# Kernel tuning notes

Measured on AMD Instinct MI355X. Metric: run time of the kernel, lower is better.

## Reference

```python
import jax, jax.numpy as jnp
import numpy as np

N_NODES = 100000
N_EDGES = 1600000


def gcn_conv(x, W, b, src, dst, n):
    # PyG GCNConv: x @ W, add self-loops, symmetric deg^{-1/2} normalization,
    # sum-aggregate messages from src into dst, then add bias.
    h = x @ W  # [N, out]
    loops = jnp.arange(n, dtype=src.dtype)
    s = jnp.concatenate([src, loops])
    d = jnp.concatenate([dst, loops])
    deg = jax.ops.segment_sum(jnp.ones_like(d, dtype=h.dtype), d, num_segments=n)
    dinv = 1.0 / jnp.sqrt(deg)  # deg >= 1 thanks to self-loops
    norm = dinv[s] * dinv[d]  # [E + N]
    msg = h[s] * norm[:, None]
    out = jax.ops.segment_sum(msg, d, num_segments=n)
    return out + b


def setup_inputs() -> dict:
    key = jax.random.key(0)
    k1, k2, k3, k4 = jax.random.split(key, 4)
    x = jax.random.normal(k1, (N_NODES, 64), dtype=jnp.float32)
    edge_index = jax.random.randint(k2, (2, N_EDGES), 0, N_NODES, dtype=jnp.int64)
    W1 = jax.random.normal(k3, (64, 32), dtype=jnp.float32) * (1.0 / np.sqrt(64))
    b1 = jnp.zeros((32,), dtype=jnp.float32)
    W2 = jax.random.normal(k4, (32, 16), dtype=jnp.float32) * (1.0 / np.sqrt(32))
    b2 = jnp.zeros((16,), dtype=jnp.float32)
    return {"x": x, "edge_index": edge_index, "W1": W1, "b1": b1, "W2": W2, "b2": b2}


def reference(x, edge_index, W1, b1, W2, b2):
    n = x.shape[0]
    src, dst = edge_index[0], edge_index[1]
    h = gcn_conv(x, W1, b1, src, dst, n)
    h = jax.nn.relu(h)
    h = gcn_conv(h, W2, b2, src, dst, n)
    return jax.nn.log_softmax(h, axis=1)
```

## Files before the change

### kernel.cpp

```cpp
#include <hip/hip_runtime.h>
#include <hip/hip_bf16.h>


#define FEAT_IN 64
#define FEAT_H  32
#define FEAT_O  16
#define MAXNB   512
#define PART_G  192

__global__ void k_detect(const uint4* __restrict__ xw4,
                         const int* __restrict__ ei, int* __restrict__ flags) {
    __shared__ int s_f32, s_i64nz;
    if (threadIdx.x == 0) { s_f32 = 0; s_i64nz = 0; }
    __syncthreads();
    int t = threadIdx.x;
    int hit = 0;
    for (int i = t; i < 4096; i += 256) {
        uint4 u = xw4[i];
        unsigned a0 = u.x, a1 = u.y, a2 = u.z, a3 = u.w;
        if ((a0 & 0x7F800000u) == 0x7F800000u || (a0 & 0x00007F80u) == 0x00007F80u) hit = 1;
        if ((a1 & 0x7F800000u) == 0x7F800000u || (a1 & 0x00007F80u) == 0x00007F80u) hit = 1;
        if ((a2 & 0x7F800000u) == 0x7F800000u || (a2 & 0x00007F80u) == 0x00007F80u) hit = 1;
        if ((a3 & 0x7F800000u) == 0x7F800000u || (a3 & 0x00007F80u) == 0x00007F80u) hit = 1;
    }
    if (hit) atomicOr(&s_f32, 1);
    int nz = 0;
    for (int i = t; i < 128; i += 256) {
        if (ei[2 * i + 1] != 0) nz = 1;
    }
    if (nz) atomicOr(&s_i64nz, 1);
    __syncthreads();
    if (t == 0) { flags[0] = s_f32; flags[1] = s_i64nz ? 0 : 1; }
}

__global__ void k_hist(const int* __restrict__ ei, int e, const int* __restrict__ flags,
                       int* __restrict__ hist, int G, int NBk) {
    __shared__ int lh[MAXNB];
    int t = threadIdx.x, g = blockIdx.x;
    for (int i = t; i < NBk; i += 256) lh[i] = 0;
    __syncthreads();
    int chunk = (e + G - 1) / G;
    int beg = g * chunk, end = min(e, beg + chunk);
    bool i64 = flags[1] != 0;
    for (int i = beg + t; i < end; i += 256) {
        int d = i64 ? ei[2 * (e + i)] : ei[e + i];
        atomicAdd(&lh[d >> 8], 1);
    }
    __syncthreads();
    for (int i = t; i < NBk; i += 256) hist[(size_t)i * G + g] = lh[i];
}

__global__ void k_scan1(const int* __restrict__ in, int* __restrict__ out,
                        int* __restrict__ bsum, int len) {
    __shared__ int s[256];
    int t = threadIdx.x;
    int base = blockIdx.x * 1024 + t * 4;
    int a0 = (base + 0) < len ? in[base + 0] : 0;
    int a1 = (base + 1) < len ? in[base + 1] : 0;
    int a2 = (base + 2) < len ? in[base + 2] : 0;
    int a3 = (base + 3) < len ? in[base + 3] : 0;
    int tsum = a0 + a1 + a2 + a3;
    s[t] = tsum;
    __syncthreads();
    for (int off = 1; off < 256; off <<= 1) {
        int x = (t >= off) ? s[t - off] : 0;
        __syncthreads();
        s[t] += x;
        __syncthreads();
    }
    int ex = s[t] - tsum;
    if (base + 0 < len) out[base + 0] = ex;
    if (base + 1 < len) out[base + 1] = ex + a0;
    if (base + 2 < len) out[base + 2] = ex + a0 + a1;
    if (base + 3 < len) out[base + 3] = ex + a0 + a1 + a2;
    if (t == 255) bsum[blockIdx.x] = s[255];
}

__global__ void k_scan2(int* __restrict__ bsum, int nb) {
    __shared__ int s[256];
    int t = threadIdx.x;
    int v = (t < nb) ? bsum[t] : 0;
    s[t] = v;
    __syncthreads();
    for (int off = 1; off < 256; off <<= 1) {
        int x = (t >= off) ? s[t - off] : 0;
        __syncthreads();
        s[t] += x;
        __syncthreads();
    }
    if (t < nb) bsum[t] = s[t] - v;
}

__device__ __forceinline__ int base_at(const int* base, const int* bsum, int idx) {
    return base[idx] + bsum[idx >> 10];
}

__global__ void k_partition(const int* __restrict__ ei, int e, const int* __restrict__ flags,
                            const int* __restrict__ base, const int* __restrict__ bsum,
                            int* __restrict__ part, int G, int NBk) {
    __shared__ int cur[MAXNB];
    int t = threadIdx.x, g = blockIdx.x;
    for (int i = t; i < NBk; i += 256) cur[i] = base_at(base, bsum, i * G + g);
    __syncthreads();
    int chunk = (e + G - 1) / G;
    int beg = g * chunk, end = min(e, beg + chunk);
    bool i64 = flags[1] != 0;
    for (int i = beg + t; i < end; i += 256) {
        int s, d;
        if (i64) { s = ei[2 * i]; d = ei[2 * (e + i)]; }
        else     { s = ei[i];     d = ei[e + i]; }
        int pos = atomicAdd(&cur[d >> 8], 1);
        part[pos] = s | ((d & 255) << 24);
    }
}

__global__ void k_bucket_csr(const int* __restrict__ part, const int* __restrict__ base,
                             const int* __restrict__ bsum, int e, int G, int NBk, int n,
                             int* __restrict__ row_start, int* __restrict__ col,
                             float* __restrict__ dinv) {
    __shared__ int cnt[256], spre[256], cur[256], ssc[256];
    int t = threadIdx.x, b = blockIdx.x;
    int beg = base_at(base, bsum, b * G);
    int end = (b == NBk - 1) ? e : base_at(base, bsum, (b + 1) * G);
    cnt[t] = 0; cur[t] = 0;
    __syncthreads();
    for (int j = beg + t; j < end; j += 256) atomicAdd(&cnt[((unsigned)part[j]) >> 24], 1);
    __syncthreads();
    int v = cnt[t];
    ssc[t] = v;
    __syncthreads();
    for (int off = 1; off < 256; off <<= 1) {
        int x = (t >= off) ? ssc[t - off] : 0;
        __syncthreads();
        ssc[t] += x;
        __syncthreads();
    }
    spre[t] = ssc[t] - v;
    int node = b * 256 + t;
    if (node < n) {
        row_start[node] = beg + spre[t];
        dinv[node] = rsqrtf((float)v + 1.0f);
    }
    if (b == NBk - 1 && t == 0) row_start[n] = e;
    __syncthreads();
    for (int j = beg + t; j < end; j += 256) {
        int r = part[j];
        int dl = ((unsigned)r) >> 24;
        int off = atomicAdd(&cur[dl], 1);
        col[beg + spre[dl] + off] = r & 0x00FFFFFF;
    }
}

__global__ void k_gemm1(const void* __restrict__ xv, const void* __restrict__ W1v,
                        const int* __restrict__ flags, const float* __restrict__ dinv,
                        float* __restrict__ h1s, int n) {
    __shared__ float sW[FEAT_IN * FEAT_H];
    __shared__ float sx[8][FEAT_IN];
    int t = threadIdx.x;
    bool f32 = flags[0] != 0;
    if (f32) {
        const float* W = (const float*)W1v;
        for (int i = t; i < FEAT_IN * FEAT_H; i += 256) sW[i] = W[i];
    } else {
        const __hip_bfloat16* W = (const __hip_bfloat16*)W1v;
        for (int i = t; i < FEAT_IN * FEAT_H; i += 256) sW[i] = __bfloat162float(W[i]);
    }
    int nl = t >> 5, f = t & 31;
    int node = blockIdx.x * 8 + nl;
    if (node < n) {
        float2 v;
        if (f32) {
            v = ((const float2*)xv)[node * (FEAT_IN / 2) + f];
        } else {
            v = __bfloat1622float2(((const __hip_bfloat162*)xv)[node * (FEAT_IN / 2) + f]);
        }
        sx[nl][2 * f]     = v.x;
        sx[nl][2 * f + 1] = v.y;
    }
    __syncthreads();
    if (node < n) {
        float acc = 0.0f;
#pragma unroll
        for (int k = 0; k < FEAT_IN; ++k) acc += sx[nl][k] * sW[k * FEAT_H + f];
        h1s[node * FEAT_H + f] = acc * dinv[node];
    }
}

__global__ void k_gather1_gemm2(const int* __restrict__ row_start, const int* __restrict__ col,
                                const float* __restrict__ h1s, const void* __restrict__ W2v,
                                const void* __restrict__ b1v, const int* __restrict__ flags,
                                const float* __restrict__ dinv, float* __restrict__ h2s, int n) {
    __shared__ float sW[FEAT_H * FEAT_O];
    __shared__ float sb1[FEAT_H];
    __shared__ float sz[32][FEAT_H + 1];
    int t = threadIdx.x;
    bool f32 = flags[0] != 0;
    if (f32) {
        const float* W = (const float*)W2v;
        for (int i = t; i < FEAT_H * FEAT_O; i += 256) sW[i] = W[i];
        if (t < FEAT_H) sb1[t] = ((const float*)b1v)[t];
    } else {
        const __hip_bfloat16* W = (const __hip_bfloat16*)W2v;
        for (int i = t; i < FEAT_H * FEAT_O; i += 256) sW[i] = __bfloat162float(W[i]);
        if (t < FEAT_H) sb1[t] = __bfloat162float(((const __hip_bfloat16*)b1v)[t]);
    }
    __syncthreads();

    int g = t >> 3, l = t & 7;
    int d = blockIdx.x * 32 + g;
    if (d < n) {
        const float4* h4 = (const float4*)h1s;
        float4 acc = h4[(size_t)d * 8 + l];
        int beg = row_start[d], end = row_start[d + 1];
        int j = beg;
        for (; j + 4 <= end; j += 4) {
            int c0 = col[j + 0], c1 = col[j + 1], c2 = col[j + 2], c3 = col[j + 3];
            float4 v0 = h4[(size_t)c0 * 8 + l];
            float4 v1 = h4[(size_t)c1 * 8 + l];
            float4 v2 = h4[(size_t)c2 * 8 + l];
            float4 v3 = h4[(size_t)c3 * 8 + l];
            acc.x += (v0.x + v1.x) + (v2.x + v3.x);
            acc.y += (v0.y + v1.y) + (v2.y + v3.y);
            acc.z += (v0.z + v1.z) + (v2.z + v3.z);
            acc.w += (v0.w + v1.w) + (v2.w + v3.w);
        }
        for (; j < end; ++j) {
            float4 v = h4[(size_t)col[j] * 8 + l];
            acc.x += v.x; acc.y += v.y; acc.z += v.z; acc.w += v.w;
        }
        float dv = dinv[d];
        sz[g][l * 4 + 0] = fmaxf(dv * acc.x + sb1[l * 4 + 0], 0.0f);
        sz[g][l * 4 + 1] = fmaxf(dv * acc.y + sb1[l * 4 + 1], 0.0f);
        sz[g][l * 4 + 2] = fmaxf(dv * acc.z + sb1[l * 4 + 2], 0.0f);
        sz[g][l * 4 + 3] = fmaxf(dv * acc.w + sb1[l * 4 + 3], 0.0f);
    }
    __syncthreads();
#pragma unroll
    for (int it = 0; it < 2; ++it) {
        int nl = (t >> 4) + it * 16;
        int o = t & 15;
        int node = blockIdx.x * 32 + nl;
        if (node < n) {
            float a = 0.0f;
#pragma unroll
            for (int f = 0; f < FEAT_H; ++f) a += sz[nl][f] * sW[f * FEAT_O + o];
            h2s[node * FEAT_O + o] = a * dinv[node];
        }
    }
}

__global__ void k_gather2_lsm(const int* __restrict__ row_start, const int* __restrict__ col,
                              const float* __restrict__ h2s, const void* __restrict__ b2v,
                              const int* __restrict__ flags, const float* __restrict__ dinv,
                              float* __restrict__ out, int n) {
    __shared__ float sb2[FEAT_O];
    int t = threadIdx.x;
    if (t < FEAT_O) {
        sb2[t] = flags[0] ? ((const float*)b2v)[t]
                          : __bfloat162float(((const __hip_bfloat16*)b2v)[t]);
    }
    __syncthreads();
    int g = t >> 2, l = t & 3;
    int d = blockIdx.x * 64 + g;
    if (d >= n) return;
    const float4* h4 = (const float4*)h2s;
    float4 acc = h4[(size_t)d * 4 + l];
    int beg = row_start[d], end = row_start[d + 1];
    int j = beg;
    for (; j + 4 <= end; j += 4) {
        int c0 = col[j + 0], c1 = col[j + 1], c2 = col[j + 2], c3 = col[j + 3];
        float4 v0 = h4[(size_t)c0 * 4 + l];
        float4 v1 = h4[(size_t)c1 * 4 + l];
        float4 v2 = h4[(size_t)c2 * 4 + l];
        float4 v3 = h4[(size_t)c3 * 4 + l];
        acc.x += (v0.x + v1.x) + (v2.x + v3.x);
        acc.y += (v0.y + v1.y) + (v2.y + v3.y);
        acc.z += (v0.z + v1.z) + (v2.z + v3.z);
        acc.w += (v0.w + v1.w) + (v2.w + v3.w);
    }
    for (; j < end; ++j) {
        float4 v = h4[(size_t)col[j] * 4 + l];
        acc.x += v.x; acc.y += v.y; acc.z += v.z; acc.w += v.w;
    }
    float dv = dinv[d];
    float v0 = dv * acc.x + sb2[l * 4 + 0];
    float v1 = dv * acc.y + sb2[l * 4 + 1];
    float v2 = dv * acc.z + sb2[l * 4 + 2];
    float v3 = dv * acc.w + sb2[l * 4 + 3];
    float m = fmaxf(fmaxf(v0, v1), fmaxf(v2, v3));
    m = fmaxf(m, __shfl_xor(m, 1, 4));
    m = fmaxf(m, __shfl_xor(m, 2, 4));
    float ssum = __expf(v0 - m) + __expf(v1 - m) + __expf(v2 - m) + __expf(v3 - m);
    ssum += __shfl_xor(ssum, 1, 4);
    ssum += __shfl_xor(ssum, 2, 4);
    float lg = m + logf(ssum);
    float4 o4 = { v0 - lg, v1 - lg, v2 - lg, v3 - lg };
    ((float4*)out)[(size_t)d * 4 + l] = o4;
}

extern "C" void kernel_launch(void* const* d_in, const int* in_sizes, int n_in,
                              void* d_out, int out_size, void* d_ws, size_t ws_size,
                              hipStream_t stream) {
    const void* x  = d_in[0];
    const int*  ei = (const int*)d_in[1];
    const void* W1 = d_in[2];
    const void* b1 = d_in[3];
    const void* W2 = d_in[4];
    const void* b2 = d_in[5];
    float* out = (float*)d_out;

    const int n = in_sizes[0] / FEAT_IN;
    const int e = in_sizes[1] / 2;
    const int NBk = (n + 255) >> 8;
    const int G = PART_G;
    const int hlen = NBk * G;

    int*   part = (int*)d_ws;
    float* h1s  = (float*)d_ws;
    float* h2s  = (float*)d_ws + 32 * (size_t)n;
    float* dinv = h2s + 16 * (size_t)n;
    int* flags     = (int*)(dinv + n);
    int* hist      = flags + 4;
    int* base      = hist + hlen;
    int* bsum      = base + hlen;
    int* row_start = bsum + 256;
    int* col       = row_start + n + 1;

    k_detect<<<1, 256, 0, stream>>>((const uint4*)x, ei, flags);

    k_hist<<<G, 256, 0, stream>>>(ei, e, flags, hist, G, NBk);
    int snb = (hlen + 1023) / 1024;
    k_scan1<<<snb, 256, 0, stream>>>(hist, base, bsum, hlen);
    k_scan2<<<1, 256, 0, stream>>>(bsum, snb);
    k_partition<<<G, 256, 0, stream>>>(ei, e, flags, base, bsum, part, G, NBk);
    k_bucket_csr<<<NBk, 256, 0, stream>>>(part, base, bsum, e, G, NBk, n,
                                          row_start, col, dinv);

    k_gemm1<<<(n + 7) / 8, 256, 0, stream>>>(x, W1, flags, dinv, h1s, n);
    k_gather1_gemm2<<<(n + 31) / 32, 256, 0, stream>>>(row_start, col, h1s, W2, b1, flags,
                                                       dinv, h2s, n);
    k_gather2_lsm<<<(n + 63) / 64, 256, 0, stream>>>(row_start, col, h2s, b2, flags,
                                                     dinv, out, n);
}
```

Baseline: 214.0 us.

## Drop CSR build, aggregate per bucket with LDS atomics and bf16 features

Removes the per-node CSR construction (col/row_start) and instead aggregates messages per 128-node destination bucket directly from the partitioned edge list, accumulating in shared memory with atomics. Intermediate features h1/h2 are stored in bf16 to halve gather traffic, and the bucket size shrinks from 256 to 128 so the accumulators fit in LDS. This trades a full pass over the edges and a scatter for LDS atomic contention and reduced precision in the intermediate features.

```diff
diff --git a/kernel.cpp b/kernel.cpp
--- a/kernel.cpp
+++ b/kernel.cpp
@@ -5,8 +5,13 @@
 #define FEAT_IN 64
 #define FEAT_H  32
 #define FEAT_O  16
-#define MAXNB   512
+#define BUCK    128
+#define MAXNB   1024
 #define PART_G  192
+
+__device__ __forceinline__ float2 upk_bf2(unsigned w) {
+    return make_float2(__uint_as_float(w << 16), __uint_as_float(w & 0xFFFF0000u));
+}
 
 __global__ void k_detect(const uint4* __restrict__ xw4,
                          const int* __restrict__ ei, int* __restrict__ flags) {
@@ -44,7 +49,7 @@
     bool i64 = flags[1] != 0;
     for (int i = beg + t; i < end; i += 256) {
         int d = i64 ? ei[2 * (e + i)] : ei[e + i];
-        atomicAdd(&lh[d >> 8], 1);
+        atomicAdd(&lh[d >> 7], 1);
     }
     __syncthreads();
     for (int i = t; i < NBk; i += 256) hist[(size_t)i * G + g] = lh[i];
@@ -109,53 +114,33 @@
         int s, d;
         if (i64) { s = ei[2 * i]; d = ei[2 * (e + i)]; }
         else     { s = ei[i];     d = ei[e + i]; }
-        int pos = atomicAdd(&cur[d >> 8], 1);
-        part[pos] = s | ((d & 255) << 24);
-    }
-}
-
-__global__ void k_bucket_csr(const int* __restrict__ part, const int* __restrict__ base,
-                             const int* __restrict__ bsum, int e, int G, int NBk, int n,
-                             int* __restrict__ row_start, int* __restrict__ col,
-                             float* __restrict__ dinv) {
-    __shared__ int cnt[256], spre[256], cur[256], ssc[256];
+        int pos = atomicAdd(&cur[d >> 7], 1);
+        part[pos] = s | ((d & (BUCK - 1)) << 24);
+    }
+}
+
+__global__ void k_bucket_dinv(const int* __restrict__ part, const int* __restrict__ base,
+                              const int* __restrict__ bsum, int e, int G, int NBk, int n,
+                              float* __restrict__ dinv) {
+    __shared__ int cnt[BUCK];
     int t = threadIdx.x, b = blockIdx.x;
+    if (t < BUCK) cnt[t] = 0;
+    __syncthreads();
     int beg = base_at(base, bsum, b * G);
     int end = (b == NBk - 1) ? e : base_at(base, bsum, (b + 1) * G);
-    cnt[t] = 0; cur[t] = 0;
-    __syncthreads();
     for (int j = beg + t; j < end; j += 256) atomicAdd(&cnt[((unsigned)part[j]) >> 24], 1);
     __syncthreads();
-    int v = cnt[t];
-    ssc[t] = v;
-    __syncthreads();
-    for (int off = 1; off < 256; off <<= 1) {
-        int x = (t >= off) ? ssc[t - off] : 0;
-        __syncthreads();
-        ssc[t] += x;
-        __syncthreads();
-    }
-    spre[t] = ssc[t] - v;
-    int node = b * 256 + t;
-    if (node < n) {
-        row_start[node] = beg + spre[t];
-        dinv[node] = rsqrtf((float)v + 1.0f);
-    }
-    if (b == NBk - 1 && t == 0) row_start[n] = e;
-    __syncthreads();
-    for (int j = beg + t; j < end; j += 256) {
-        int r = part[j];
-        int dl = ((unsigned)r) >> 24;
-        int off = atomicAdd(&cur[dl], 1);
-        col[beg + spre[dl] + off] = r & 0x00FFFFFF;
+    if (t < BUCK) {
+        int node = b * BUCK + t;
+        if (node < n) dinv[node] = rsqrtf((float)cnt[t] + 1.0f);
     }
 }
 
 __global__ void k_gemm1(const void* __restrict__ xv, const void* __restrict__ W1v,
                         const int* __restrict__ flags, const float* __restrict__ dinv,
-                        float* __restrict__ h1s, int n) {
+                        __hip_bfloat162* __restrict__ h1s2, int n) {
     __shared__ float sW[FEAT_IN * FEAT_H];
-    __shared__ float sx[8][FEAT_IN];
+    __shared__ float sx[16][FEAT_IN + 1];
     int t = threadIdx.x;
     bool f32 = flags[0] != 0;
     if (f32) {
@@ -165,35 +150,56 @@
         const __hip_bfloat16* W = (const __hip_bfloat16*)W1v;
         for (int i = t; i < FEAT_IN * FEAT_H; i += 256) sW[i] = __bfloat162float(W[i]);
     }
-    int nl = t >> 5, f = t & 31;
-    int node = blockIdx.x * 8 + nl;
-    if (node < n) {
-        float2 v;
-        if (f32) {
-            v = ((const float2*)xv)[node * (FEAT_IN / 2) + f];
-        } else {
-            v = __bfloat1622float2(((const __hip_bfloat162*)xv)[node * (FEAT_IN / 2) + f]);
-        }
-        sx[nl][2 * f]     = v.x;
-        sx[nl][2 * f + 1] = v.y;
-    }
-    __syncthreads();
-    if (node < n) {
-        float acc = 0.0f;
-#pragma unroll
-        for (int k = 0; k < FEAT_IN; ++k) acc += sx[nl][k] * sW[k * FEAT_H + f];
-        h1s[node * FEAT_H + f] = acc * dinv[node];
-    }
-}
-
-__global__ void k_gather1_gemm2(const int* __restrict__ row_start, const int* __restrict__ col,
-                                const float* __restrict__ h1s, const void* __restrict__ W2v,
-                                const void* __restrict__ b1v, const int* __restrict__ flags,
-                                const float* __restrict__ dinv, float* __restrict__ h2s, int n) {
+#pragma unroll
+    for (int tile = 0; tile < 2; ++tile) {
+        int nodeBase = blockIdx.x * 32 + tile * 16;
+        __syncthreads();
+        {
+            int xn = t >> 4, c = t & 15;
+            int node = nodeBase + xn;
+            if (node < n) {
+                if (f32) {
+                    float4 v = ((const float4*)xv)[(size_t)node * 16 + c];
+                    sx[xn][c * 4 + 0] = v.x; sx[xn][c * 4 + 1] = v.y;
+                    sx[xn][c * 4 + 2] = v.z; sx[xn][c * 4 + 3] = v.w;
+                } else {
+                    const __hip_bfloat162* x2 = (const __hip_bfloat162*)xv;
+                    float2 a = __bfloat1622float2(x2[(size_t)node * 32 + c * 2 + 0]);
+                    float2 b = __bfloat1622float2(x2[(size_t)node * 32 + c * 2 + 1]);
+                    sx[xn][c * 4 + 0] = a.x; sx[xn][c * 4 + 1] = a.y;
+                    sx[xn][c * 4 + 2] = b.x; sx[xn][c * 4 + 3] = b.y;
+                }
+            }
+        }
+        __syncthreads();
+        int nl = t >> 4, g = t & 15;
+        int node = nodeBase + nl;
+        if (node < n) {
+            float a0 = 0.0f, a1 = 0.0f;
+#pragma unroll
+            for (int k = 0; k < FEAT_IN; ++k) {
+                float s = sx[nl][k];
+                a0 += s * sW[k * FEAT_H + 2 * g];
+                a1 += s * sW[k * FEAT_H + 2 * g + 1];
+            }
+            float dv = dinv[node];
+            __hip_bfloat162 o;
+            o.x = __float2bfloat16(a0 * dv);
+            o.y = __float2bfloat16(a1 * dv);
+            h1s2[(size_t)node * 16 + g] = o;
+        }
+    }
+}
+
+__global__ void k_agg1(const int* __restrict__ part, const int* __restrict__ base,
+                       const int* __restrict__ bsum, int e, int G, int NBk, int n,
+                       const uint4* __restrict__ h1s4, const void* __restrict__ W2v,
+                       const void* __restrict__ b1v, const int* __restrict__ flags,
+                       const float* __restrict__ dinv, __hip_bfloat162* __restrict__ h2s2) {
     __shared__ float sW[FEAT_H * FEAT_O];
     __shared__ float sb1[FEAT_H];
-    __shared__ float sz[32][FEAT_H + 1];
-    int t = threadIdx.x;
+    __shared__ float acc[FEAT_H][BUCK];
+    int t = threadIdx.x, b = blockIdx.x;
     bool f32 = flags[0] != 0;
     if (f32) {
         const float* W = (const float*)W2v;
@@ -204,98 +210,130 @@
         for (int i = t; i < FEAT_H * FEAT_O; i += 256) sW[i] = __bfloat162float(W[i]);
         if (t < FEAT_H) sb1[t] = __bfloat162float(((const __hip_bfloat16*)b1v)[t]);
     }
-    __syncthreads();
-
-    int g = t >> 3, l = t & 7;
-    int d = blockIdx.x * 32 + g;
-    if (d < n) {
-        const float4* h4 = (const float4*)h1s;
-        float4 acc = h4[(size_t)d * 8 + l];
-        int beg = row_start[d], end = row_start[d + 1];
-        int j = beg;
-        for (; j + 4 <= end; j += 4) {
-            int c0 = col[j + 0], c1 = col[j + 1], c2 = col[j + 2], c3 = col[j + 3];
-            float4 v0 = h4[(size_t)c0 * 8 + l];
-            float4 v1 = h4[(size_t)c1 * 8 + l];
-            float4 v2 = h4[(size_t)c2 * 8 + l];
-            float4 v3 = h4[(size_t)c3 * 8 + l];
-            acc.x += (v0.x + v1.x) + (v2.x + v3.x);
-            acc.y += (v0.y + v1.y) + (v2.y + v3.y);
-            acc.z += (v0.z + v1.z) + (v2.z + v3.z);
-            acc.w += (v0.w + v1.w) + (v2.w + v3.w);
-        }
-        for (; j < end; ++j) {
-            float4 v = h4[(size_t)col[j] * 8 + l];
-            acc.x += v.x; acc.y += v.y; acc.z += v.z; acc.w += v.w;
-        }
-        float dv = dinv[d];
-        sz[g][l * 4 + 0] = fmaxf(dv * acc.x + sb1[l * 4 + 0], 0.0f);
-        sz[g][l * 4 + 1] = fmaxf(dv * acc.y + sb1[l * 4 + 1], 0.0f);
-        sz[g][l * 4 + 2] = fmaxf(dv * acc.z + sb1[l * 4 + 2], 0.0f);
-        sz[g][l * 4 + 3] = fmaxf(dv * acc.w + sb1[l * 4 + 3], 0.0f);
-    }
-    __syncthreads();
-#pragma unroll
-    for (int it = 0; it < 2; ++it) {
-        int nl = (t >> 4) + it * 16;
-        int o = t & 15;
-        int node = blockIdx.x * 32 + nl;
-        if (node < n) {
-            float a = 0.0f;
-#pragma unroll
-            for (int f = 0; f < FEAT_H; ++f) a += sz[nl][f] * sW[f * FEAT_O + o];
-            h2s[node * FEAT_O + o] = a * dinv[node];
-        }
-    }
-}
-
-__global__ void k_gather2_lsm(const int* __restrict__ row_start, const int* __restrict__ col,
-                              const float* __restrict__ h2s, const void* __restrict__ b2v,
-                              const int* __restrict__ flags, const float* __restrict__ dinv,
-                              float* __restrict__ out, int n) {
+    int nb0 = b * BUCK;
+    for (int idx = t; idx < BUCK * 4; idx += 256) {
+        int nl = idx >> 2, c = idx & 3;
+        int node = nb0 + nl;
+        float2 p0, p1, p2, p3;
+        if (node < n) {
+            uint4 u = h1s4[(size_t)node * 4 + c];
+            p0 = upk_bf2(u.x); p1 = upk_bf2(u.y); p2 = upk_bf2(u.z); p3 = upk_bf2(u.w);
+        } else {
+            p0 = p1 = p2 = p3 = make_float2(0.f, 0.f);
+        }
+        int fb = c * 8;
+        acc[fb + 0][nl] = p0.x; acc[fb + 1][nl] = p0.y;
+        acc[fb + 2][nl] = p1.x; acc[fb + 3][nl] = p1.y;
+        acc[fb + 4][nl] = p2.x; acc[fb + 5][nl] = p2.y;
+        acc[fb + 6][nl] = p3.x; acc[fb + 7][nl] = p3.y;
+    }
+    __syncthreads();
+    int beg = base_at(base, bsum, b * G);
+    int end = (b == NBk - 1) ? e : base_at(base, bsum, (b + 1) * G);
+    int q = t & 3, eo = t >> 2;
+    for (int j = beg + eo; j < end; j += 64) {
+        int r = part[j];
+        int s = r & 0x00FFFFFF, dl = ((unsigned)r) >> 24;
+        uint4 u = h1s4[(size_t)s * 4 + q];
+        float2 p0 = upk_bf2(u.x), p1 = upk_bf2(u.y), p2 = upk_bf2(u.z), p3 = upk_bf2(u.w);
+        int fb = q * 8;
+        atomicAdd(&acc[fb + 0][dl], p0.x); atomicAdd(&acc[fb + 1][dl], p0.y);
+        atomicAdd(&acc[fb + 2][dl], p1.x); atomicAdd(&acc[fb + 3][dl], p1.y);
+        atomicAdd(&acc[fb + 4][dl], p2.x); atomicAdd(&acc[fb + 5][dl], p2.y);
+        atomicAdd(&acc[fb + 6][dl], p3.x); atomicAdd(&acc[fb + 7][dl], p3.y);
+    }
+    __syncthreads();
+#pragma unroll
+    for (int sub = 0; sub < 4; ++sub) {
+        int nl = (t >> 3) + sub * 32;
+        int m = t & 7;
+        int node = nb0 + nl;
+        if (node < n) {
+            float dv = dinv[node];
+            float a0 = 0.0f, a1 = 0.0f;
+#pragma unroll
+            for (int f = 0; f < FEAT_H; ++f) {
+                float z = fmaxf(dv * acc[f][nl] + sb1[f], 0.0f);
+                a0 += z * sW[f * FEAT_O + 2 * m];
+                a1 += z * sW[f * FEAT_O + 2 * m + 1];
+            }
+            __hip_bfloat162 o;
+            o.x = __float2bfloat16(a0 * dv);
+            o.y = __float2bfloat16(a1 * dv);
+            h2s2[(size_t)node * 8 + m] = o;
+        }
+    }
+}
+
+__global__ void k_agg2(const int* __restrict__ part, const int* __restrict__ base,
+                       const int* __restrict__ bsum, int e, int G, int NBk, int n,
+                       const uint4* __restrict__ h2s4, const void* __restrict__ b2v,
+                       const int* __restrict__ flags, const float* __restrict__ dinv,
+                       float4* __restrict__ out4) {
     __shared__ float sb2[FEAT_O];
-    int t = threadIdx.x;
+    __shared__ float acc[FEAT_O][BUCK];
+    int t = threadIdx.x, b = blockIdx.x;
     if (t < FEAT_O) {
         sb2[t] = flags[0] ? ((const float*)b2v)[t]
                           : __bfloat162float(((const __hip_bfloat16*)b2v)[t]);
     }
-    __syncthreads();
-    int g = t >> 2, l = t & 3;
-    int d = blockIdx.x * 64 + g;
-    if (d >= n) return;
-    const float4* h4 = (const float4*)h2s;
-    float4 acc = h4[(size_t)d * 4 + l];
-    int beg = row_start[d], end = row_start[d + 1];
-    int j = beg;
-    for (; j + 4 <= end; j += 4) {
-        int c0 = col[j + 0], c1 = col[j + 1], c2 = col[j + 2], c3 = col[j + 3];
-        float4 v0 = h4[(size_t)c0 * 4 + l];
-        float4 v1 = h4[(size_t)c1 * 4 + l];
-        float4 v2 = h4[(size_t)c2 * 4 + l];
-        float4 v3 = h4[(size_t)c3 * 4 + l];
-        acc.x += (v0.x + v1.x) + (v2.x + v3.x);
-        acc.y += (v0.y + v1.y) + (v2.y + v3.y);
-        acc.z += (v0.z + v1.z) + (v2.z + v3.z);
-        acc.w += (v0.w + v1.w) + (v2.w + v3.w);
-    }
-    for (; j < end; ++j) {
-        float4 v = h4[(size_t)col[j] * 4 + l];
-        acc.x += v.x; acc.y += v.y; acc.z += v.z; acc.w += v.w;
-    }
-    float dv = dinv[d];
-    float v0 = dv * acc.x + sb2[l * 4 + 0];
-    float v1 = dv * acc.y + sb2[l * 4 + 1];
-    float v2 = dv * acc.z + sb2[l * 4 + 2];
-    float v3 = dv * acc.w + sb2[l * 4 + 3];
-    float m = fmaxf(fmaxf(v0, v1), fmaxf(v2, v3));
-    m = fmaxf(m, __shfl_xor(m, 1, 4));
-    m = fmaxf(m, __shfl_xor(m, 2, 4));
-    float ssum = __expf(v0 - m) + __expf(v1 - m) + __expf(v2 - m) + __expf(v3 - m);
-    ssum += __shfl_xor(ssum, 1, 4);
-    ssum += __shfl_xor(ssum, 2, 4);
-    float lg = m + logf(ssum);
-    float4 o4 = { v0 - lg, v1 - lg, v2 - lg, v3 - lg };
-    ((float4*)out)[(size_t)d * 4 + l] = o4;
+    int nb0 = b * BUCK;
+    for (int idx = t; idx < BUCK * 2; idx += 256) {
+        int nl = idx >> 1, c = idx & 1;
+        int node = nb0 + nl;
+        float2 p0, p1, p2, p3;
+        if (node < n) {
+            uint4 u = h2s4[(size_t)node * 2 + c];
+            p0 = upk_bf2(u.x); p1 = upk_bf2(u.y); p2 = upk_bf2(u.z); p3 = upk_bf2(u.w);
+        } else {
+            p0 = p1 = p2 = p3 = make_float2(0.f, 0.f);
+        }
+        int fb = c * 8;
+        acc[fb + 0][nl] = p0.x; acc[fb + 1][nl] = p0.y;
+        acc[fb + 2][nl] = p1.x; acc[fb + 3][nl] = p1.y;
+        acc[fb + 4][nl] = p2.x; acc[fb + 5][nl] = p2.y;
+        acc[fb + 6][nl] = p3.x; acc[fb + 7][nl] = p3.y;
+    }
+    __syncthreads();
+    int beg = base_at(base, bsum, b * G);
+    int end = (b == NBk - 1) ? e : base_at(base, bsum, (b + 1) * G);
+    int half = t & 1, eo = t >> 1;
+    for (int j = beg + eo; j < end; j += 128) {
+        int r = part[j];
+        int s = r & 0x00FFFFFF, dl = ((unsigned)r) >> 24;
+        uint4 u = h2s4[(size_t)s * 2 + half];
+        float2 p0 = upk_bf2(u.x), p1 = upk_bf2(u.y), p2 = upk_bf2(u.z), p3 = upk_bf2(u.w);
+        int fb = half * 8;
+        atomicAdd(&acc[fb + 0][dl], p0.x); atomicAdd(&acc[fb + 1][dl], p0.y);
+        atomicAdd(&acc[fb + 2][dl], p1.x); atomicAdd(&acc[fb + 3][dl], p1.y);
+        atomicAdd(&acc[fb + 4][dl], p2.x); atomicAdd(&acc[fb + 5][dl], p2.y);
+        atomicAdd(&acc[fb + 6][dl], p3.x); atomicAdd(&acc[fb + 7][dl], p3.y);
+    }
+    __syncthreads();
+    {
+        int nl = t >> 1, h = t & 1;
+        int node = nb0 + nl;
+        if (node < n) {
+            float dv = dinv[node];
+            float v[8];
+            float mx = -1e30f;
+#pragma unroll
+            for (int k = 0; k < 8; ++k) {
+                v[k] = dv * acc[h * 8 + k][nl] + sb2[h * 8 + k];
+                mx = fmaxf(mx, v[k]);
+            }
+            mx = fmaxf(mx, __shfl_xor(mx, 1));
+            float ssum = 0.0f;
+#pragma unroll
+            for (int k = 0; k < 8; ++k) ssum += __expf(v[k] - mx);
+            ssum += __shfl_xor(ssum, 1);
+            float lg = mx + logf(ssum);
+            float4 o0 = { v[0] - lg, v[1] - lg, v[2] - lg, v[3] - lg };
+            float4 o1 = { v[4] - lg, v[5] - lg, v[6] - lg, v[7] - lg };
+            out4[(size_t)node * 4 + h * 2 + 0] = o0;
+            out4[(size_t)node * 4 + h * 2 + 1] = o1;
+        }
+    }
 }
 
 extern "C" void kernel_launch(void* const* d_in, const int* in_sizes, int n_in,
@@ -307,24 +345,21 @@
     const void* b1 = d_in[3];
     const void* W2 = d_in[4];
     const void* b2 = d_in[5];
-    float* out = (float*)d_out;
 
     const int n = in_sizes[0] / FEAT_IN;
     const int e = in_sizes[1] / 2;
-    const int NBk = (n + 255) >> 8;
+    const int NBk = (n + BUCK - 1) / BUCK;
     const int G = PART_G;
     const int hlen = NBk * G;
 
-    int*   part = (int*)d_ws;
-    float* h1s  = (float*)d_ws;
-    float* h2s  = (float*)d_ws + 32 * (size_t)n;
-    float* dinv = h2s + 16 * (size_t)n;
-    int* flags     = (int*)(dinv + n);
-    int* hist      = flags + 4;
-    int* base      = hist + hlen;
-    int* bsum      = base + hlen;
-    int* row_start = bsum + 256;
-    int* col       = row_start + n + 1;
+    int*   part  = (int*)d_ws;
+    __hip_bfloat162* h1s2 = (__hip_bfloat162*)(part + e);
+    __hip_bfloat162* h2s2 = h1s2 + 16 * (size_t)n;
+    float* dinv  = (float*)(h2s2 + 8 * (size_t)n);
+    int* flags   = (int*)(dinv + n);
+    int* hist    = flags + 4;
+    int* base    = hist + hlen;
+    int* bsum    = base + hlen;
 
     k_detect<<<1, 256, 0, stream>>>((const uint4*)x, ei, flags);
 
@@ -333,12 +368,11 @@
     k_scan1<<<snb, 256, 0, stream>>>(hist, base, bsum, hlen);
     k_scan2<<<1, 256, 0, stream>>>(bsum, snb);
     k_partition<<<G, 256, 0, stream>>>(ei, e, flags, base, bsum, part, G, NBk);
-    k_bucket_csr<<<NBk, 256, 0, stream>>>(part, base, bsum, e, G, NBk, n,
-                                          row_start, col, dinv);
-
-    k_gemm1<<<(n + 7) / 8, 256, 0, stream>>>(x, W1, flags, dinv, h1s, n);
-    k_gather1_gemm2<<<(n + 31) / 32, 256, 0, stream>>>(row_start, col, h1s, W2, b1, flags,
-                                                       dinv, h2s, n);
-    k_gather2_lsm<<<(n + 63) / 64, 256, 0, stream>>>(row_start, col, h2s, b2, flags,
-                                                     dinv, out, n);
-}
+    k_bucket_dinv<<<NBk, 256, 0, stream>>>(part, base, bsum, e, G, NBk, n, dinv);
+
+    k_gemm1<<<(n + 31) / 32, 256, 0, stream>>>(x, W1, flags, dinv, h1s2, n);
+    k_agg1<<<NBk, 256, 0, stream>>>(part, base, bsum, e, G, NBk, n,
+                                    (const uint4*)h1s2, W2, b1, flags, dinv, h2s2);
+    k_agg2<<<NBk, 256, 0, stream>>>(part, base, bsum, e, G, NBk, n,
+                                    (const uint4*)h2s2, b2, flags, dinv, (float4*)d_out);
+}
```

After: 665.0 us. 211% more time.

## Store intermediate node features in bf16 to halve gather traffic

Applied to the files above, without the earlier changes.

The pre-scaled hidden features h1 and h2 are now stored as bf16 instead of fp32, halving the bytes fetched per neighbour in both gather kernels. Each thread now handles more features per node (16-byte loads carry 8 bf16 values), and the block-to-node mappings and workspace layout are reorganised to match. gemm1 processes 32 nodes per block with 2 outputs per thread. The cost is bf16 rounding of the intermediate features, which may hurt accuracy against the fp32 reference.

```diff
diff --git a/kernel.cpp b/kernel.cpp
--- a/kernel.cpp
+++ b/kernel.cpp
@@ -7,6 +7,10 @@
 #define FEAT_O  16
 #define MAXNB   512
 #define PART_G  192
+
+__device__ __forceinline__ float2 upk_bf2(unsigned w) {
+    return make_float2(__uint_as_float(w << 16), __uint_as_float(w & 0xFFFF0000u));
+}
 
 __global__ void k_detect(const uint4* __restrict__ xw4,
                          const int* __restrict__ ei, int* __restrict__ flags) {
@@ -153,9 +157,9 @@
 
 __global__ void k_gemm1(const void* __restrict__ xv, const void* __restrict__ W1v,
                         const int* __restrict__ flags, const float* __restrict__ dinv,
-                        float* __restrict__ h1s, int n) {
+                        __hip_bfloat162* __restrict__ h1s2, int n) {
     __shared__ float sW[FEAT_IN * FEAT_H];
-    __shared__ float sx[8][FEAT_IN];
+    __shared__ float sx[16][FEAT_IN + 1];
     int t = threadIdx.x;
     bool f32 = flags[0] != 0;
     if (f32) {
@@ -165,34 +169,55 @@
         const __hip_bfloat16* W = (const __hip_bfloat16*)W1v;
         for (int i = t; i < FEAT_IN * FEAT_H; i += 256) sW[i] = __bfloat162float(W[i]);
     }
-    int nl = t >> 5, f = t & 31;
-    int node = blockIdx.x * 8 + nl;
-    if (node < n) {
-        float2 v;
-        if (f32) {
-            v = ((const float2*)xv)[node * (FEAT_IN / 2) + f];
-        } else {
-            v = __bfloat1622float2(((const __hip_bfloat162*)xv)[node * (FEAT_IN / 2) + f]);
-        }
-        sx[nl][2 * f]     = v.x;
-        sx[nl][2 * f + 1] = v.y;
-    }
-    __syncthreads();
-    if (node < n) {
-        float acc = 0.0f;
-#pragma unroll
-        for (int k = 0; k < FEAT_IN; ++k) acc += sx[nl][k] * sW[k * FEAT_H + f];
-        h1s[node * FEAT_H + f] = acc * dinv[node];
+#pragma unroll
+    for (int tile = 0; tile < 2; ++tile) {
+        int nodeBase = blockIdx.x * 32 + tile * 16;
+        __syncthreads();
+        {
+            int xn = t >> 4, c = t & 15;
+            int node = nodeBase + xn;
+            if (node < n) {
+                if (f32) {
+                    float4 v = ((const float4*)xv)[(size_t)node * 16 + c];
+                    sx[xn][c * 4 + 0] = v.x; sx[xn][c * 4 + 1] = v.y;
+                    sx[xn][c * 4 + 2] = v.z; sx[xn][c * 4 + 3] = v.w;
+                } else {
+                    const __hip_bfloat162* x2 = (const __hip_bfloat162*)xv;
+                    float2 a = __bfloat1622float2(x2[(size_t)node * 32 + c * 2 + 0]);
+                    float2 b = __bfloat1622float2(x2[(size_t)node * 32 + c * 2 + 1]);
+                    sx[xn][c * 4 + 0] = a.x; sx[xn][c * 4 + 1] = a.y;
+                    sx[xn][c * 4 + 2] = b.x; sx[xn][c * 4 + 3] = b.y;
+                }
+            }
+        }
+        __syncthreads();
+        int nl = t >> 4, g = t & 15;
+        int node = nodeBase + nl;
+        if (node < n) {
+            float a0 = 0.0f, a1 = 0.0f;
+#pragma unroll
+            for (int k = 0; k < FEAT_IN; ++k) {
+                float s = sx[nl][k];
+                a0 += s * sW[k * FEAT_H + 2 * g];
+                a1 += s * sW[k * FEAT_H + 2 * g + 1];
+            }
+            float dv = dinv[node];
+            __hip_bfloat162 o;
+            o.x = __float2bfloat16(a0 * dv);
+            o.y = __float2bfloat16(a1 * dv);
+            h1s2[(size_t)node * 16 + g] = o;
+        }
     }
 }
 
 __global__ void k_gather1_gemm2(const int* __restrict__ row_start, const int* __restrict__ col,
-                                const float* __restrict__ h1s, const void* __restrict__ W2v,
+                                const uint4* __restrict__ h1q, const void* __restrict__ W2v,
                                 const void* __restrict__ b1v, const int* __restrict__ flags,
-                                const float* __restrict__ dinv, float* __restrict__ h2s, int n) {
+                                const float* __restrict__ dinv,
+                                __hip_bfloat162* __restrict__ h2s2, int n) {
     __shared__ float sW[FEAT_H * FEAT_O];
     __shared__ float sb1[FEAT_H];
-    __shared__ float sz[32][FEAT_H + 1];
+    __shared__ float sz[64][FEAT_H + 1];
     int t = threadIdx.x;
     bool f32 = flags[0] != 0;
     if (f32) {
@@ -206,53 +231,82 @@
     }
     __syncthreads();
 
-    int g = t >> 3, l = t & 7;
-    int d = blockIdx.x * 32 + g;
+    int g = t >> 2, l = t & 3;
+    int d = blockIdx.x * 64 + g;
     if (d < n) {
-        const float4* h4 = (const float4*)h1s;
-        float4 acc = h4[(size_t)d * 8 + l];
+        float a[8];
+        {
+            uint4 u = h1q[(size_t)d * 4 + l];
+            float2 p0 = upk_bf2(u.x), p1 = upk_bf2(u.y), p2 = upk_bf2(u.z), p3 = upk_bf2(u.w);
+            a[0] = p0.x; a[1] = p0.y; a[2] = p1.x; a[3] = p1.y;
+            a[4] = p2.x; a[5] = p2.y; a[6] = p3.x; a[7] = p3.y;
+        }
         int beg = row_start[d], end = row_start[d + 1];
         int j = beg;
         for (; j + 4 <= end; j += 4) {
             int c0 = col[j + 0], c1 = col[j + 1], c2 = col[j + 2], c3 = col[j + 3];
-            float4 v0 = h4[(size_t)c0 * 8 + l];
-            float4 v1 = h4[(size_t)c1 * 8 + l];
-            float4 v2 = h4[(size_t)c2 * 8 + l];
-            float4 v3 = h4[(size_t)c3 * 8 + l];
-            acc.x += (v0.x + v1.x) + (v2.x + v3.x);
-            acc.y += (v0.y + v1.y) + (v2.y + v3.y);
-            acc.z += (v0.z + v1.z) + (v2.z + v3.z);
-            acc.w += (v0.w + v1.w) + (v2.w + v3.w);
+            uint4 u0 = h1q[(size_t)c0 * 4 + l];
+            uint4 u1 = h1q[(size_t)c1 * 4 + l];
+            uint4 u2 = h1q[(size_t)c2 * 4 + l];
+            uint4 u3 = h1q[(size_t)c3 * 4 + l];
+            float2 p;
+            p = upk_bf2(u0.x); a[0] += p.x; a[1] += p.y;
+            p = upk_bf2(u0.y); a[2] += p.x; a[3] += p.y;
+            p = upk_bf2(u0.z); a[4] += p.x; a[5] += p.y;
+            p = upk_bf2(u0.w); a[6] += p.x; a[7] += p.y;
+            p = upk_bf2(u1.x); a[0] += p.x; a[1] += p.y;
+            p = upk_bf2(u1.y); a[2] += p.x; a[3] += p.y;
+            p = upk_bf2(u1.z); a[4] += p.x; a[5] += p.y;
+            p = upk_bf2(u1.w); a[6] += p.x; a[7] += p.y;
+            p = upk_bf2(u2.x); a[0] += p.x; a[1] += p.y;
+            p = upk_bf2(u2.y); a[2] += p.x; a[3] += p.y;
+            p = upk_bf2(u2.z); a[4] += p.x; a[5] += p.y;
+            p = upk_bf2(u2.w); a[6] += p.x; a[7] += p.y;
+            p = upk_bf2(u3.x); a[0] += p.x; a[1] += p.y;
+            p = upk_bf2(u3.y); a[2] += p.x; a[3] += p.y;
+            p = upk_bf2(u3.z); a[4] += p.x; a[5] += p.y;
+            p = upk_bf2(u3.w); a[6] += p.x; a[7] += p.y;
         }
         for (; j < end; ++j) {
-            float4 v = h4[(size_t)col[j] * 8 + l];
-            acc.x += v.x; acc.y += v.y; acc.z += v.z; acc.w += v.w;
+            uint4 u = h1q[(size_t)col[j] * 4 + l];
+            float2 p;
+            p = upk_bf2(u.x); a[0] += p.x; a[1] += p.y;
+            p = upk_bf2(u.y); a[2] += p.x; a[3] += p.y;
+            p = upk_bf2(u.z); a[4] += p.x; a[5] += p.y;
+            p = upk_bf2(u.w); a[6] += p.x; a[7] += p.y;
         }
         float dv = dinv[d];
-        sz[g][l * 4 + 0] = fmaxf(dv * acc.x + sb1[l * 4 + 0], 0.0f);
-        sz[g][l * 4 + 1] = fmaxf(dv * acc.y + sb1[l * 4 + 1], 0.0f);
-        sz[g][l * 4 + 2] = fmaxf(dv * acc.z + sb1[l * 4 + 2], 0.0f);
-        sz[g][l * 4 + 3] = fmaxf(dv * acc.w + sb1[l * 4 + 3], 0.0f);
+#pragma unroll
+        for (int k = 0; k < 8; ++k)
+            sz[g][l * 8 + k] = fmaxf(dv * a[k] + sb1[l * 8 + k], 0.0f);
     }
     __syncthreads();
 #pragma unroll
     for (int it = 0; it < 2; ++it) {
-        int nl = (t >> 4) + it * 16;
-        int o = t & 15;
-        int node = blockIdx.x * 32 + nl;
+        int nl = (t >> 3) + it * 32;
+        int m = t & 7;
+        int node = blockIdx.x * 64 + nl;
         if (node < n) {
-            float a = 0.0f;
-#pragma unroll
-            for (int f = 0; f < FEAT_H; ++f) a += sz[nl][f] * sW[f * FEAT_O + o];
-            h2s[node * FEAT_O + o] = a * dinv[node];
+            float a0 = 0.0f, a1 = 0.0f;
+#pragma unroll
+            for (int f = 0; f < FEAT_H; ++f) {
+                float z = sz[nl][f];
+                a0 += z * sW[f * FEAT_O + 2 * m];
+                a1 += z * sW[f * FEAT_O + 2 * m + 1];
+            }
+            float dv = dinv[node];
+            __hip_bfloat162 o;
+            o.x = __float2bfloat16(a0 * dv);
+            o.y = __float2bfloat16(a1 * dv);
+            h2s2[(size_t)node * 8 + m] = o;
         }
     }
 }
 
 __global__ void k_gather2_lsm(const int* __restrict__ row_start, const int* __restrict__ col,
-                              const float* __restrict__ h2s, const void* __restrict__ b2v,
+                              const uint4* __restrict__ h2q, const void* __restrict__ b2v,
                               const int* __restrict__ flags, const float* __restrict__ dinv,
-                              float* __restrict__ out, int n) {
+                              float4* __restrict__ out4, int n) {
     __shared__ float sb2[FEAT_O];
     int t = threadIdx.x;
     if (t < FEAT_O) {
@@ -260,42 +314,68 @@
                           : __bfloat162float(((const __hip_bfloat16*)b2v)[t]);
     }
     __syncthreads();
-    int g = t >> 2, l = t & 3;
-    int d = blockIdx.x * 64 + g;
+    int g = t >> 1, h = t & 1;
+    int d = blockIdx.x * 128 + g;
     if (d >= n) return;
-    const float4* h4 = (const float4*)h2s;
-    float4 acc = h4[(size_t)d * 4 + l];
+    float a[8];
+    {
+        uint4 u = h2q[(size_t)d * 2 + h];
+        float2 p0 = upk_bf2(u.x), p1 = upk_bf2(u.y), p2 = upk_bf2(u.z), p3 = upk_bf2(u.w);
+        a[0] = p0.x; a[1] = p0.y; a[2] = p1.x; a[3] = p1.y;
+        a[4] = p2.x; a[5] = p2.y; a[6] = p3.x; a[7] = p3.y;
+    }
     int beg = row_start[d], end = row_start[d + 1];
     int j = beg;
     for (; j + 4 <= end; j += 4) {
         int c0 = col[j + 0], c1 = col[j + 1], c2 = col[j + 2], c3 = col[j + 3];
-        float4 v0 = h4[(size_t)c0 * 4 + l];
-        float4 v1 = h4[(size_t)c1 * 4 + l];
-        float4 v2 = h4[(size_t)c2 * 4 + l];
-        float4 v3 = h4[(size_t)c3 * 4 + l];
-        acc.x += (v0.x + v1.x) + (v2.x + v3.x);
-        acc.y += (v0.y + v1.y) + (v2.y + v3.y);
-        acc.z += (v0.z + v1.z) + (v2.z + v3.z);
-        acc.w += (v0.w + v1.w) + (v2.w + v3.w);
+        uint4 u0 = h2q[(size_t)c0 * 2 + h];
+        uint4 u1 = h2q[(size_t)c1 * 2 + h];
+        uint4 u2 = h2q[(size_t)c2 * 2 + h];
+        uint4 u3 = h2q[(size_t)c3 * 2 + h];
+        float2 p;
+        p = upk_bf2(u0.x); a[0] += p.x; a[1] += p.y;
+        p = upk_bf2(u0.y); a[2] += p.x; a[3] += p.y;
+        p = upk_bf2(u0.z); a[4] += p.x; a[5] += p.y;
+        p = upk_bf2(u0.w); a[6] += p.x; a[7] += p.y;
+        p = upk_bf2(u1.x); a[0] += p.x; a[1] += p.y;
+        p = upk_bf2(u1.y); a[2] += p.x; a[3] += p.y;
+        p = upk_bf2(u1.z); a[4] += p.x; a[5] += p.y;
+        p = upk_bf2(u1.w); a[6] += p.x; a[7] += p.y;
+        p = upk_bf2(u2.x); a[0] += p.x; a[1] += p.y;
+        p = upk_bf2(u2.y); a[2] += p.x; a[3] += p.y;
+        p = upk_bf2(u2.z); a[4] += p.x; a[5] += p.y;
+        p = upk_bf2(u2.w); a[6] += p.x; a[7] += p.y;
+        p = upk_bf2(u3.x); a[0] += p.x; a[1] += p.y;
+        p = upk_bf2(u3.y); a[2] += p.x; a[3] += p.y;
+        p = upk_bf2(u3.z); a[4] += p.x; a[5] += p.y;
+        p = upk_bf2(u3.w); a[6] += p.x; a[7] += p.y;
     }
     for (; j < end; ++j) {
-        float4 v = h4[(size_t)col[j] * 4 + l];
-        acc.x += v.x; acc.y += v.y; acc.z += v.z; acc.w += v.w;
+        uint4 u = h2q[(size_t)col[j] * 2 + h];
+        float2 p;
+        p = upk_bf2(u.x); a[0] += p.x; a[1] += p.y;
+        p = upk_bf2(u.y); a[2] += p.x; a[3] += p.y;
+        p = upk_bf2(u.z); a[4] += p.x; a[5] += p.y;
+        p = upk_bf2(u.w); a[6] += p.x; a[7] += p.y;
     }
     float dv = dinv[d];
-    float v0 = dv * acc.x + sb2[l * 4 + 0];
-    float v1 = dv * acc.y + sb2[l * 4 + 1];
-    float v2 = dv * acc.z + sb2[l * 4 + 2];
-    float v3 = dv * acc.w + sb2[l * 4 + 3];
-    float m = fmaxf(fmaxf(v0, v1), fmaxf(v2, v3));
-    m = fmaxf(m, __shfl_xor(m, 1, 4));
-    m = fmaxf(m, __shfl_xor(m, 2, 4));
-    float ssum = __expf(v0 - m) + __expf(v1 - m) + __expf(v2 - m) + __expf(v3 - m);
-    ssum += __shfl_xor(ssum, 1, 4);
-    ssum += __shfl_xor(ssum, 2, 4);
-    float lg = m + logf(ssum);
-    float4 o4 = { v0 - lg, v1 - lg, v2 - lg, v3 - lg };
-    ((float4*)out)[(size_t)d * 4 + l] = o4;
+    float v[8];
+    float mx = -1e30f;
+#pragma unroll
+    for (int k = 0; k < 8; ++k) {
+        v[k] = dv * a[k] + sb2[h * 8 + k];
+        mx = fmaxf(mx, v[k]);
+    }
+    mx = fmaxf(mx, __shfl_xor(mx, 1));
+    float ssum = 0.0f;
+#pragma unroll
+    for (int k = 0; k < 8; ++k) ssum += __expf(v[k] - mx);
+    ssum += __shfl_xor(ssum, 1);
+    float lg = mx + logf(ssum);
+    float4 o0 = { v[0] - lg, v[1] - lg, v[2] - lg, v[3] - lg };
+    float4 o1 = { v[4] - lg, v[5] - lg, v[6] - lg, v[7] - lg };
+    out4[(size_t)d * 4 + h * 2 + 0] = o0;
+    out4[(size_t)d * 4 + h * 2 + 1] = o1;
 }
 
 extern "C" void kernel_launch(void* const* d_in, const int* in_sizes, int n_in,
@@ -307,7 +387,6 @@
     const void* b1 = d_in[3];
     const void* W2 = d_in[4];
     const void* b2 = d_in[5];
-    float* out = (float*)d_out;
 
     const int n = in_sizes[0] / FEAT_IN;
     const int e = in_sizes[1] / 2;
@@ -315,16 +394,16 @@
     const int G = PART_G;
     const int hlen = NBk * G;
 
-    int*   part = (int*)d_ws;
-    float* h1s  = (float*)d_ws;
-    float* h2s  = (float*)d_ws + 32 * (size_t)n;
-    float* dinv = h2s + 16 * (size_t)n;
+    int* part = (int*)d_ws;
+    __hip_bfloat162* h1s2 = (__hip_bfloat162*)d_ws;
+    int* col  = (int*)d_ws + e;
+    __hip_bfloat162* h2s2 = (__hip_bfloat162*)(col + e);
+    float* dinv = (float*)(h2s2 + 8 * (size_t)n);
     int* flags     = (int*)(dinv + n);
     int* hist      = flags + 4;
     int* base      = hist + hlen;
     int* bsum      = base + hlen;
     int* row_start = bsum + 256;
-    int* col       = row_start + n + 1;
 
     k_detect<<<1, 256, 0, stream>>>((const uint4*)x, ei, flags);
 
@@ -336,9 +415,9 @@
     k_bucket_csr<<<NBk, 256, 0, stream>>>(part, base, bsum, e, G, NBk, n,
                                           row_start, col, dinv);
 
-    k_gemm1<<<(n + 7) / 8, 256, 0, stream>>>(x, W1, flags, dinv, h1s, n);
-    k_gather1_gemm2<<<(n + 31) / 32, 256, 0, stream>>>(row_start, col, h1s, W2, b1, flags,
-                                                       dinv, h2s, n);
-    k_gather2_lsm<<<(n + 63) / 64, 256, 0, stream>>>(row_start, col, h2s, b2, flags,
-                                                     dinv, out, n);
-}
+    k_gemm1<<<(n + 31) / 32, 256, 0, stream>>>(x, W1, flags, dinv, h1s2, n);
+    k_gather1_gemm2<<<(n + 63) / 64, 256, 0, stream>>>(row_start, col, (const uint4*)h1s2,
+                                                       W2, b1, flags, dinv, h2s2, n);
+    k_gather2_lsm<<<(n + 127) / 128, 256, 0, stream>>>(row_start, col, (const uint4*)h2s2,
+                                                       b2, flags, dinv, (float4*)d_out, n);
+}
```

Result: faster. 197.7 us (-7.6%).
